# Kernel optimization log

Hardware: AMD Instinct MI355X
Metric: run time of the kernel (lower is better)

## Reference

```python
import jax, jax.numpy as jnp
import numpy as np

N = 50000      # nodes
E = 800000     # edges
P = 200000     # link pairs
D_IN = 128     # input_dim
F_NUM = 128    # filter_num
OUT = 2        # out_dim
K = 10         # APPNP propagation steps
ALPHA = 0.1    # teleport prob


def setup_inputs() -> dict:
    key = jax.random.key(0)
    ks = jax.random.split(key, 9)
    x = jax.random.normal(ks[0], (N, D_IN), dtype=jnp.float32)
    edge_index = jax.random.randint(ks[1], (2, E), 0, N)
    index = jax.random.randint(ks[2], (P, 2), 0, N)
    s1 = 1.0 / np.sqrt(D_IN)
    s2 = 1.0 / np.sqrt(F_NUM)
    s3 = 1.0 / np.sqrt(2 * F_NUM)
    W1 = jax.random.uniform(ks[3], (F_NUM, D_IN), minval=-s1, maxval=s1)
    b1 = jax.random.uniform(ks[4], (F_NUM,), minval=-s1, maxval=s1)
    W2 = jax.random.uniform(ks[5], (F_NUM, F_NUM), minval=-s2, maxval=s2)
    b2 = jax.random.uniform(ks[6], (F_NUM,), minval=-s2, maxval=s2)
    W3 = jax.random.uniform(ks[7], (OUT, 2 * F_NUM), minval=-s3, maxval=s3)
    b3 = jax.random.uniform(ks[8], (OUT,), minval=-s3, maxval=s3)
    return {"x": x, "edge_index": edge_index, "index": index,
            "W1": W1, "b1": b1, "W2": W2, "b2": b2, "W3": W3, "b3": b3}


def _gcn_norm(edge_index, num_nodes):
    # PyG gcn_norm: add self-loops, sym norm D^{-1/2} (A+I) D^{-1/2}
    src, dst = edge_index[0], edge_index[1]
    loop = jnp.arange(num_nodes, dtype=src.dtype)
    src = jnp.concatenate([src, loop])
    dst = jnp.concatenate([dst, loop])
    deg = jax.ops.segment_sum(jnp.ones_like(src, dtype=jnp.float32), dst,
                              num_segments=num_nodes)
    dinv = jnp.where(deg > 0, jax.lax.rsqrt(deg), 0.0)
    norm = dinv[src] * dinv[dst]  # [E+N]
    return src, dst, norm


def _appnp(x, src, dst, norm, num_nodes):
    # h_{k+1} = (1-alpha) * A_hat h_k + alpha * x0
    def step(h, _):
        agg = jax.ops.segment_sum(norm[:, None] * h[src], dst,
                                  num_segments=num_nodes)
        return (1.0 - ALPHA) * agg + ALPHA * x, None
    h, _ = jax.lax.scan(step, x, None, length=K)
    return h


def reference(x, edge_index, index, W1, b1, W2, b2, W3, b3):
    num_nodes = x.shape[0]
    src, dst, norm = _gcn_norm(edge_index, num_nodes)
    h = x @ W1.T + b1                      # [N, F]
    h = jax.nn.relu(_appnp(h, src, dst, norm, num_nodes))
    h = h @ W2.T + b2                      # [N, F]
    h = jax.nn.relu(_appnp(h, src, dst, norm, num_nodes))
    feat = jnp.concatenate([h[index[:, 0]], h[index[:, 1]]], axis=-1)  # [P, 2F]
    out = feat @ W3.T + b3                 # [P, OUT]
    return jax.nn.log_softmax(out, axis=1)
```

## Files before the change

### kernel.cpp

```cpp
#include <hip/hip_runtime.h>
#include <math.h>

#define NN 50000
#define NE 800000
#define NP 200000
#define NF 128
#define NNP (NN + 1)
#define NEDGE_TOT (NE + NN)
#define NBLK 196
#define NBK 64
#define DPB 782
#define BKCAP 16384
#define EPB 2048
#define NSL 4
#define SF 32
#define NCPAD 1000064

typedef __attribute__((ext_vector_type(8))) short short8;
typedef __attribute__((ext_vector_type(4))) float float4v;
typedef __attribute__((ext_vector_type(2))) _Float16 h2;

__device__ __forceinline__ unsigned short f2bf(float f) {
    unsigned u = __float_as_uint(f);
    return (unsigned short)((u + 0x7fffu + ((u >> 16) & 1u)) >> 16);
}
__device__ __forceinline__ unsigned pack2bf(float a, float b) {
    return (unsigned)f2bf(a) | ((unsigned)f2bf(b) << 16);
}

__device__ __forceinline__ h2 u2h2(unsigned u) {
    union { unsigned u; h2 h; } c; c.u = u; return c.h;
}
__device__ __forceinline__ unsigned h22u(h2 h) {
    union { unsigned u; h2 h; } c; c.h = h; return c.u;
}
__device__ __forceinline__ float h_lo(unsigned u) { return (float)u2h2(u).x; }
__device__ __forceinline__ float h_hi(unsigned u) { return (float)u2h2(u).y; }
__device__ __forceinline__ unsigned pack2h(float a, float b) {
    h2 h; h.x = (_Float16)a; h.y = (_Float16)b; return h22u(h);
}

__global__ __launch_bounds__(256) void init_cnt_k(int* __restrict__ cnt,
                                                  float4* __restrict__ puv) {
    int i = blockIdx.x * 256 + threadIdx.x;
    if (i < NN) {
        cnt[i] = 1;
        puv[i] = make_float4(0.f, 0.f, 0.f, 0.f);
    }
}

__global__ __launch_bounds__(256) void count_k(const int* __restrict__ ei,
                                               int* __restrict__ cnt) {
    int e = blockIdx.x * 256 + threadIdx.x;
    if (e < NE) atomicAdd(&cnt[ei[NE + e]], 1);
}

__global__ __launch_bounds__(256) void scan_reduce_k(const int* __restrict__ cnt,
                                                     int* __restrict__ bsum,
                                                     float* __restrict__ dinv) {
    __shared__ int s[256];
    int t = threadIdx.x;
    int idx = blockIdx.x * 256 + t;
    int v = (idx < NN) ? cnt[idx] : 0;
    if (idx < NN) dinv[idx] = rsqrtf((float)v);
    int vp = (v + 3) & ~3;
    s[t] = vp;
    __syncthreads();
    for (int off = 128; off > 0; off >>= 1) {
        if (t < off) s[t] += s[t + off];
        __syncthreads();
    }
    if (t == 0) bsum[blockIdx.x] = s[0];
}

__global__ __launch_bounds__(256) void scan_bsums_k(const int* __restrict__ bsum,
                                                    int* __restrict__ boff) {
    __shared__ int s[256];
    int t = threadIdx.x;
    int v = (t < NBLK) ? bsum[t] : 0;
    s[t] = v;
    __syncthreads();
    for (int off = 1; off < 256; off <<= 1) {
        int add = (t >= off) ? s[t - off] : 0;
        __syncthreads();
        s[t] += add;
        __syncthreads();
    }
    if (t < NBLK) boff[t] = s[t] - v;
}

__global__ __launch_bounds__(256) void scan_down_k(const int* __restrict__ cnt,
                                                   const int* __restrict__ boff,
                                                   int* __restrict__ row_ptr) {
    __shared__ int s[256];
    int t = threadIdx.x;
    int idx = blockIdx.x * 256 + t;
    int v = (idx < NN) ? ((cnt[idx] + 3) & ~3) : 0;
    s[t] = v;
    __syncthreads();
    for (int off = 1; off < 256; off <<= 1) {
        int add = (t >= off) ? s[t - off] : 0;
        __syncthreads();
        s[t] += add;
        __syncthreads();
    }
    int excl = s[t] - v + boff[blockIdx.x] + 4;
    if (idx < NN) {
        row_ptr[idx] = excl;
        if (idx == NN - 1) row_ptr[NN] = excl + v;
    }
}

__global__ __launch_bounds__(256) void fill_cols_k(unsigned* __restrict__ colsu) {
    int t = blockIdx.x * 256 + threadIdx.x;
    if (t < NCPAD / 2) colsu[t] = (unsigned)NN | ((unsigned)NN << 16);
}

__global__ __launch_bounds__(256) void bin_k(const int* __restrict__ ei,
                                             int* __restrict__ gtail,
                                             int2* __restrict__ gbk) {
    __shared__ int cntA[NBK], baseA[NBK], gposA[NBK];
    __shared__ int2 stage[EPB];
    int tid = threadIdx.x;
    int ebase = blockIdx.x * EPB;
    int sv[8], dv[8], lp8[8], bk8[8];
    bool val[8];
    if (tid < NBK) cntA[tid] = 0;
    __syncthreads();
#pragma unroll
    for (int k = 0; k < 8; ++k) {
        int e = ebase + k * 256 + tid;
        val[k] = (e < NEDGE_TOT);
        if (val[k]) {
            int s, d;
            if (e < NE) { s = ei[e]; d = ei[NE + e]; }
            else        { s = d = e - NE; }
            sv[k] = s; dv[k] = d;
            bk8[k] = d / DPB;
            lp8[k] = atomicAdd(&cntA[bk8[k]], 1);
        }
    }
    __syncthreads();
    if (tid == 0) {
        int run = 0;
        for (int b = 0; b < NBK; ++b) { baseA[b] = run; run += cntA[b]; }
    }
    __syncthreads();
    if (tid < NBK && cntA[tid] > 0)
        gposA[tid] = atomicAdd(&gtail[tid], cntA[tid]);
    __syncthreads();
#pragma unroll
    for (int k = 0; k < 8; ++k)
        if (val[k]) {
            int2 r; r.x = sv[k]; r.y = dv[k];
            stage[baseA[bk8[k]] + lp8[k]] = r;
        }
    __syncthreads();
    int total = baseA[NBK - 1] + cntA[NBK - 1];
    for (int i = tid; i < total; i += 256) {
        int2 r = stage[i];
        int b = r.y / DPB;
        gbk[(size_t)b * BKCAP + gposA[b] + (i - baseA[b])] = r;
    }
}

__global__ __launch_bounds__(256) void build_k(const int* __restrict__ row_ptr,
                                               const int* __restrict__ gtail,
                                               const int2* __restrict__ gbk,
                                               unsigned short* __restrict__ cols) {
    __shared__ int wcur[DPB];
    int tid = threadIdx.x;
    int b = blockIdx.x;
    int d0 = b * DPB;
    for (int i = tid; i < DPB; i += 256) {
        int d = d0 + i;
        wcur[i] = (d < NN) ? row_ptr[d] : 0;
    }
    __syncthreads();
    int nb = gtail[b];
    const int2* src = gbk + (size_t)b * BKCAP;
    for (int t = tid; t < nb; t += 256) {
        int2 r = src[t];
        int pos = atomicAdd(&wcur[r.y - d0], 1);
        cols[pos] = (unsigned short)r.x;
    }
}

__global__ __launch_bounds__(256) void zero_k(unsigned short* Ys1, unsigned short* Ys2,
                                              unsigned short* HA, unsigned short* HB,
                                              int* gtail) {
    int t = threadIdx.x;
    unsigned short* bufs[4] = {Ys1, Ys2, HA, HB};
    unsigned short* bp = bufs[t >> 6];
    int s = (t >> 4) & 3, u = t & 15;
    ((unsigned*)(bp + ((size_t)s * NNP + NN) * SF))[u] = 0u;
    if (t < NBK) gtail[t] = 0;
}

__global__ __launch_bounds__(256) void cast_w_k(const float* __restrict__ W,
                                                unsigned short* __restrict__ Wb) {
    int t = blockIdx.x * 256 + threadIdx.x;
    if (t >= 128 * 128 / 8) return;
    int i = t * 8;
    float4 f0 = *(const float4*)(W + i);
    float4 f1 = *(const float4*)(W + i + 4);
    uint4 q;
    q.x = pack2bf(f0.x, f0.y);
    q.y = pack2bf(f0.z, f0.w);
    q.z = pack2bf(f1.x, f1.y);
    q.w = pack2bf(f1.z, f1.w);
    *(uint4*)(Wb + i) = q;
}

#define GPAD 136
template <bool F32IN>
__global__ __launch_bounds__(256) void gemm_mfma_k(const void* __restrict__ Xv,
                                                   const unsigned short* __restrict__ Wb,
                                                   const float* __restrict__ bias,
                                                   const float* __restrict__ dinv,
                                                   unsigned short* __restrict__ Yu,
                                                   unsigned short* __restrict__ Ys,
                                                   int nrows) {
    __shared__ unsigned short sm[4 * 16 * GPAD];
    int wave = threadIdx.x >> 6, lane = threadIdx.x & 63;
    int rbase = blockIdx.x * 64 + wave * 16;
    if (rbase >= nrows) return;
    int quad = lane >> 4, mn = lane & 15;
    float4v acc[8];
#pragma unroll
    for (int ft = 0; ft < 8; ++ft) acc[ft] = (float4v){0.f, 0.f, 0.f, 0.f};
#pragma unroll
    for (int kb = 0; kb < 128; kb += 32) {
        short8 a;
        if (F32IN) {
            const float* X = (const float*)Xv;
            float4 f0 = *(const float4*)(X + (size_t)(rbase + mn) * NF + kb + quad * 8);
            float4 f1 = *(const float4*)(X + (size_t)(rbase + mn) * NF + kb + quad * 8 + 4);
            a[0] = (short)f2bf(f0.x); a[1] = (short)f2bf(f0.y);
            a[2] = (short)f2bf(f0.z); a[3] = (short)f2bf(f0.w);
            a[4] = (short)f2bf(f1.x); a[5] = (short)f2bf(f1.y);
            a[6] = (short)f2bf(f1.z); a[7] = (short)f2bf(f1.w);
        } else {
            const unsigned short* X = (const unsigned short*)Xv;
            a = *(const short8*)(X + (size_t)(rbase + mn) * NF + kb + quad * 8);
        }
#pragma unroll
        for (int ft = 0; ft < 8; ++ft) {
            short8 b = *(const short8*)(Wb + (size_t)(ft * 16 + mn) * NF + kb + quad * 8);
            acc[ft] = __builtin_amdgcn_mfma_f32_16x16x32_bf16(a, b, acc[ft], 0, 0, 0);
        }
    }
    unsigned short* smw = sm + wave * 16 * GPAD;
#pragma unroll
    for (int ft = 0; ft < 8; ++ft) {
        float bv = bias[ft * 16 + mn];
#pragma unroll
        for (int r = 0; r < 4; ++r) {
            union { _Float16 h; unsigned short s; } cv;
            cv.h = (_Float16)(acc[ft][r] + bv);
            smw[(quad * 4 + r) * GPAD + ft * 16 + mn] = cv.s;
        }
    }
    __syncthreads();
#pragma unroll
    for (int t = 0; t < 4; ++t) {
        int rl = t * 4 + quad;
        int row = rbase + rl;
        uint4 q = *(const uint4*)(smw + rl * GPAD + mn * 8);
        size_t sb = ((size_t)(mn >> 2) * NNP + row) * SF + (mn & 3) * 8;
        *(uint4*)(Yu + sb) = q;
        float g = dinv[row];
        uint4 qs;
        qs.x = pack2h(g * h_lo(q.x), g * h_hi(q.x));
        qs.y = pack2h(g * h_lo(q.y), g * h_hi(q.y));
        qs.z = pack2h(g * h_lo(q.z), g * h_hi(q.z));
        qs.w = pack2h(g * h_lo(q.w), g * h_hi(q.w));
        *(uint4*)(Ys + sb) = qs;
    }
}

__global__ __launch_bounds__(512) void appnp_slice_k(
    const unsigned short* __restrict__ hs,
    const unsigned short* __restrict__ x0,
    const float* __restrict__ dinv,
    unsigned short* __restrict__ out,
    const int* __restrict__ row_ptr,
    const unsigned short* __restrict__ cols,
    int mode,
    const float* __restrict__ W3,
    float* __restrict__ puv) {
    int b = blockIdx.x;
    int x = b & 7;
    int s = x & 3, hh = x >> 2;
    int wave = threadIdx.x >> 6, lane = threadIdx.x & 63;
    int g = lane >> 3, fo = lane & 7;
    int wid = (b >> 3) * 128 + hh * 64 + wave * 8 + g;
    bool valid = wid < NN;
    int nid = valid ? wid : NN;
    const unsigned short* hsS = hs + (size_t)s * NNP * SF;
    int beg = 0, dp = 0;
    if (valid) { beg = row_ptr[wid]; dp = row_ptr[wid + 1] - beg; }
    int dpm = dp;
    dpm = max(dpm, __shfl_xor(dpm, 8, 64));
    dpm = max(dpm, __shfl_xor(dpm, 16, 64));
    dpm = max(dpm, __shfl_xor(dpm, 32, 64));
    float gsc = valid ? dinv[wid] : 0.f;
    uint2 xq = *(const uint2*)(x0 + ((size_t)s * NNP + nid) * SF + fo * 4);
    h2 a01; a01.x = (_Float16)0.f; a01.y = (_Float16)0.f;
    h2 a23 = a01;
    if (dpm > 0) {
        int o0 = (0 < dp) ? beg : 0;
        int o1 = (4 < dp) ? beg + 4 : 0;
        ushort4 cq = *(const ushort4*)(cols + o0);
        ushort4 cq1 = *(const ushort4*)(cols + o1);
        uint2 q0 = *(const uint2*)(hsS + (size_t)cq.x * SF + fo * 4);
        uint2 q1 = *(const uint2*)(hsS + (size_t)cq.y * SF + fo * 4);
        uint2 q2 = *(const uint2*)(hsS + (size_t)cq.z * SF + fo * 4);
        uint2 q3 = *(const uint2*)(hsS + (size_t)cq.w * SF + fo * 4);
        for (int j = 0; j < dpm; j += 4) {
            int on = (j + 8 < dp) ? beg + j + 8 : 0;
            ushort4 cq2 = *(const ushort4*)(cols + on);
            uint2 p0 = *(const uint2*)(hsS + (size_t)cq1.x * SF + fo * 4);
            uint2 p1 = *(const uint2*)(hsS + (size_t)cq1.y * SF + fo * 4);
            uint2 p2 = *(const uint2*)(hsS + (size_t)cq1.z * SF + fo * 4);
            uint2 p3 = *(const uint2*)(hsS + (size_t)cq1.w * SF + fo * 4);
            a01 += (u2h2(q0.x) + u2h2(q1.x)) + (u2h2(q2.x) + u2h2(q3.x));
            a23 += (u2h2(q0.y) + u2h2(q1.y)) + (u2h2(q2.y) + u2h2(q3.y));
            q0 = p0; q1 = p1; q2 = p2; q3 = p3;
            cq1 = cq2;
        }
    }
    float s9 = 0.9f * gsc;
    float h0 = s9 * (float)a01.x + 0.1f * h_lo(xq.x);
    float h1 = s9 * (float)a01.y + 0.1f * h_hi(xq.x);
    float h2v = s9 * (float)a23.x + 0.1f * h_lo(xq.y);
    float h3 = s9 * (float)a23.y + 0.1f * h_hi(xq.y);
    if (mode == 0) {
        if (valid) {
            uint2 oq;
            oq.x = pack2h(gsc * h0, gsc * h1);
            oq.y = pack2h(gsc * h2v, gsc * h3);
            *(uint2*)(out + ((size_t)s * NNP + wid) * SF + fo * 4) = oq;
        }
    } else {
        h0 = fmaxf(h0, 0.f); h1 = fmaxf(h1, 0.f);
        h2v = fmaxf(h2v, 0.f); h3 = fmaxf(h3, 0.f);
        if (mode == 1) {
            if (valid) {
                uint2 oq;
                oq.x = pack2bf(h0, h1);
                oq.y = pack2bf(h2v, h3);
                *(uint2*)(out + (size_t)wid * NF + s * SF + fo * 4) = oq;
            }
        } else {
            int fb = s * SF + fo * 4;
            float4 wu0 = *(const float4*)(W3 + fb);
            float4 wv0 = *(const float4*)(W3 + 128 + fb);
            float4 wu1 = *(const float4*)(W3 + 256 + fb);
            float4 wv1 = *(const float4*)(W3 + 384 + fb);
            float du0 = h0 * wu0.x + h1 * wu0.y + h2v * wu0.z + h3 * wu0.w;
            float du1 = h0 * wu1.x + h1 * wu1.y + h2v * wu1.z + h3 * wu1.w;
            float dv0 = h0 * wv0.x + h1 * wv0.y + h2v * wv0.z + h3 * wv0.w;
            float dv1 = h0 * wv1.x + h1 * wv1.y + h2v * wv1.z + h3 * wv1.w;
            du0 += __shfl_xor(du0, 1, 64); du0 += __shfl_xor(du0, 2, 64);
            du0 += __shfl_xor(du0, 4, 64);
            du1 += __shfl_xor(du1, 1, 64); du1 += __shfl_xor(du1, 2, 64);
            du1 += __shfl_xor(du1, 4, 64);
            dv0 += __shfl_xor(dv0, 1, 64); dv0 += __shfl_xor(dv0, 2, 64);
            dv0 += __shfl_xor(dv0, 4, 64);
            dv1 += __shfl_xor(dv1, 1, 64); dv1 += __shfl_xor(dv1, 2, 64);
            dv1 += __shfl_xor(dv1, 4, 64);
            if (valid && fo < 4) {
                float v = (fo == 0) ? du0 : (fo == 1) ? du1
                          : (fo == 2) ? dv0 : dv1;
                atomicAdd(&puv[(size_t)wid * 4 + fo], v);
            }
        }
    }
}

__global__ __launch_bounds__(256) void pair2_k(const float4* __restrict__ puv,
                                               const int2* __restrict__ index,
                                               const float* __restrict__ b3,
                                               float* __restrict__ outp) {
    int p = blockIdx.x * 256 + threadIdx.x;
    if (p >= NP) return;
    int2 uv = index[p];
    float4 a = puv[uv.x];
    float4 b = puv[uv.y];
    float s0 = a.x + b.z + b3[0];
    float s1 = a.y + b.w + b3[1];
    float m = fmaxf(s0, s1);
    float lse = m + logf(expf(s0 - m) + expf(s1 - m));
    *(float2*)(outp + (size_t)p * 2) = make_float2(s0 - lse, s1 - lse);
}

extern "C" void kernel_launch(void* const* d_in, const int* in_sizes, int n_in,
                              void* d_out, int out_size, void* d_ws, size_t ws_size,
                              hipStream_t stream) {
    const float* x  = (const float*)d_in[0];
    const int* ei   = (const int*)d_in[1];
    const int* idx  = (const int*)d_in[2];
    const float* W1 = (const float*)d_in[3];
    const float* b1 = (const float*)d_in[4];
    const float* W2 = (const float*)d_in[5];
    const float* b2 = (const float*)d_in[6];
    const float* W3 = (const float*)d_in[7];
    const float* b3 = (const float*)d_in[8];
    float* out = (float*)d_out;

    char* ws = (char*)d_ws;
    size_t off = 0;
    auto alloc = [&](size_t bytes) -> void* {
        void* p = ws + off;
        off = (off + bytes + 255) & ~(size_t)255;
        return p;
    };
    const size_t HROWS = (size_t)NSL * NNP * SF;
    int*   cnt     = (int*)  alloc(NN * sizeof(int));
    float* dinv    = (float*)alloc(NN * sizeof(float));
    int*   row_ptr = (int*)  alloc((NN + 1) * sizeof(int));
    int*   bsum    = (int*)  alloc(NBLK * sizeof(int));
    int*   boff    = (int*)  alloc(NBLK * sizeof(int));
    int*   gtail   = (int*)  alloc(NBK * sizeof(int));
    int2*  gbk     = (int2*) alloc((size_t)NBK * BKCAP * sizeof(int2));
    unsigned short* cols = (unsigned short*)alloc((size_t)NCPAD * 2);
    float4* puv    = (float4*)alloc((size_t)NN * sizeof(float4));
    unsigned short* Wb1 = (unsigned short*)alloc(128 * 128 * 2);
    unsigned short* Wb2 = (unsigned short*)alloc(128 * 128 * 2);
    unsigned short* Yu1 = (unsigned short*)alloc(HROWS * 2);
    unsigned short* Ys1 = (unsigned short*)alloc(HROWS * 2);
    unsigned short* Yu2 = (unsigned short*)alloc(HROWS * 2);
    unsigned short* Ys2 = (unsigned short*)alloc(HROWS * 2);
    unsigned short* HA  = (unsigned short*)alloc(HROWS * 2);
    unsigned short* HB  = (unsigned short*)alloc(HROWS * 2);
    unsigned short* Hrelu = (unsigned short*)alloc((size_t)NN * NF * 2);

    const int gN    = (NN + 255) / 256;
    const int gE    = (NE + 255) / 256;
    const int gBin  = (NEDGE_TOT + EPB - 1) / EPB;
    const int gGemm = (NN + 63) / 64;
    const int gFill = (NCPAD / 2 + 255) / 256;
    const int gSlice = ((NN + 127) / 128) * 8;
    const int gPair = (NP + 255) / 256;

    cast_w_k<<<8, 256, 0, stream>>>(W1, Wb1);
    cast_w_k<<<8, 256, 0, stream>>>(W2, Wb2);
    zero_k<<<1, 256, 0, stream>>>(Ys1, Ys2, HA, HB, gtail);
    init_cnt_k<<<gN, 256, 0, stream>>>(cnt, puv);
    count_k<<<gE, 256, 0, stream>>>(ei, cnt);
    scan_reduce_k<<<NBLK, 256, 0, stream>>>(cnt, bsum, dinv);
    scan_bsums_k<<<1, 256, 0, stream>>>(bsum, boff);
    scan_down_k<<<NBLK, 256, 0, stream>>>(cnt, boff, row_ptr);
    fill_cols_k<<<gFill, 256, 0, stream>>>((unsigned*)cols);
    bin_k<<<gBin, 256, 0, stream>>>(ei, gtail, gbk);
    build_k<<<NBK, 256, 0, stream>>>(row_ptr, gtail, gbk, cols);

    float* puvf = (float*)puv;
    gemm_mfma_k<true><<<gGemm, 256, 0, stream>>>(x, Wb1, b1, dinv, Yu1, Ys1, NN);
    {
        const unsigned short* cur = Ys1;
        for (int k = 0; k < 10; ++k) {
            unsigned short* dst = (k == 9) ? Hrelu : ((k & 1) ? HB : HA);
            appnp_slice_k<<<gSlice, 512, 0, stream>>>(cur, Yu1, dinv, dst, row_ptr,
                                                      cols, (k == 9) ? 1 : 0, W3, puvf);
            cur = dst;
        }
    }
    gemm_mfma_k<false><<<gGemm, 256, 0, stream>>>(Hrelu, Wb2, b2, dinv, Yu2, Ys2, NN);
    {
        const unsigned short* cur = Ys2;
        for (int k = 0; k < 10; ++k) {
            unsigned short* dst = (k & 1) ? HB : HA;
            appnp_slice_k<<<gSlice, 512, 0, stream>>>(cur, Yu2, dinv, dst, row_ptr,
                                                      cols, (k == 9) ? 2 : 0, W3, puvf);
            cur = dst;
        }
    }
    pair2_k<<<gPair, 256, 0, stream>>>(puv, (const int2*)idx, b3, out);
}
```

Baseline: 827.5 us.

## Split features into 8 slices of 16 and deepen gather prefetch pipeline

Changes the feature-sliced layout from 4 slices of 32 halves to 8 slices of 16, so each node row per slice is 32 bytes. The APPNP kernel now assigns 16 nodes per wave with 4 lanes each instead of 8 nodes with 8 lanes. The gather loop prefetches two groups of neighbor rows ahead instead of one and loads the column indices with nontemporal loads. The smaller slices are meant to improve cache locality for the random gathers and raise memory-level parallelism. In exchange it uses more registers and launches a different block mapping; the edge-loop divergence now spans 16 nodes per wave.

```diff
diff --git a/kernel.cpp b/kernel.cpp
--- a/kernel.cpp
+++ b/kernel.cpp
@@ -12,13 +12,14 @@
 #define DPB 782
 #define BKCAP 16384
 #define EPB 2048
-#define NSL 4
-#define SF 32
+#define NSL 8
+#define SF 16
 #define NCPAD 1000064
 
 typedef __attribute__((ext_vector_type(8))) short short8;
 typedef __attribute__((ext_vector_type(4))) float float4v;
 typedef __attribute__((ext_vector_type(2))) _Float16 h2;
+typedef __attribute__((ext_vector_type(4))) unsigned short us4;
 
 __device__ __forceinline__ unsigned short f2bf(float f) {
     unsigned u = __float_as_uint(f);
@@ -192,7 +193,7 @@
     int t = threadIdx.x;
     unsigned short* bufs[4] = {Ys1, Ys2, HA, HB};
     unsigned short* bp = bufs[t >> 6];
-    int s = (t >> 4) & 3, u = t & 15;
+    int s = (t >> 3) & 7, u = t & 7;
     ((unsigned*)(bp + ((size_t)s * NNP + NN) * SF))[u] = 0u;
     if (t < NBK) gtail[t] = 0;
 }
@@ -267,7 +268,7 @@
         int rl = t * 4 + quad;
         int row = rbase + rl;
         uint4 q = *(const uint4*)(smw + rl * GPAD + mn * 8);
-        size_t sb = ((size_t)(mn >> 2) * NNP + row) * SF + (mn & 3) * 8;
+        size_t sb = ((size_t)(mn >> 1) * NNP + row) * SF + (mn & 1) * 8;
         *(uint4*)(Yu + sb) = q;
         float g = dinv[row];
         uint4 qs;
@@ -290,17 +291,17 @@
     const float* __restrict__ W3,
     float* __restrict__ puv) {
     int b = blockIdx.x;
-    int x = b & 7;
-    int s = x & 3, hh = x >> 2;
+    int s = b & 7;
     int wave = threadIdx.x >> 6, lane = threadIdx.x & 63;
-    int g = lane >> 3, fo = lane & 7;
-    int wid = (b >> 3) * 128 + hh * 64 + wave * 8 + g;
+    int g = lane >> 2, fo = lane & 3;
+    int wid = (b >> 3) * 128 + wave * 16 + g;
     bool valid = wid < NN;
     int nid = valid ? wid : NN;
     const unsigned short* hsS = hs + (size_t)s * NNP * SF;
     int beg = 0, dp = 0;
     if (valid) { beg = row_ptr[wid]; dp = row_ptr[wid + 1] - beg; }
     int dpm = dp;
+    dpm = max(dpm, __shfl_xor(dpm, 4, 64));
     dpm = max(dpm, __shfl_xor(dpm, 8, 64));
     dpm = max(dpm, __shfl_xor(dpm, 16, 64));
     dpm = max(dpm, __shfl_xor(dpm, 32, 64));
@@ -309,25 +310,33 @@
     h2 a01; a01.x = (_Float16)0.f; a01.y = (_Float16)0.f;
     h2 a23 = a01;
     if (dpm > 0) {
-        int o0 = (0 < dp) ? beg : 0;
-        int o1 = (4 < dp) ? beg + 4 : 0;
-        ushort4 cq = *(const ushort4*)(cols + o0);
-        ushort4 cq1 = *(const ushort4*)(cols + o1);
-        uint2 q0 = *(const uint2*)(hsS + (size_t)cq.x * SF + fo * 4);
-        uint2 q1 = *(const uint2*)(hsS + (size_t)cq.y * SF + fo * 4);
-        uint2 q2 = *(const uint2*)(hsS + (size_t)cq.z * SF + fo * 4);
-        uint2 q3 = *(const uint2*)(hsS + (size_t)cq.w * SF + fo * 4);
+        int fb4 = fo * 4;
+        auto colsat = [&](int j4) -> us4 {
+            int o = (j4 < dp) ? beg + j4 : 0;
+            return __builtin_nontemporal_load((const us4*)(cols + o));
+        };
+        us4 c0 = colsat(0);
+        us4 c1 = colsat(4);
+        us4 c2 = colsat(8);
+        uint2 A0 = *(const uint2*)(hsS + (size_t)c0.x * SF + fb4);
+        uint2 A1 = *(const uint2*)(hsS + (size_t)c0.y * SF + fb4);
+        uint2 A2 = *(const uint2*)(hsS + (size_t)c0.z * SF + fb4);
+        uint2 A3 = *(const uint2*)(hsS + (size_t)c0.w * SF + fb4);
+        uint2 B0 = *(const uint2*)(hsS + (size_t)c1.x * SF + fb4);
+        uint2 B1 = *(const uint2*)(hsS + (size_t)c1.y * SF + fb4);
+        uint2 B2 = *(const uint2*)(hsS + (size_t)c1.z * SF + fb4);
+        uint2 B3 = *(const uint2*)(hsS + (size_t)c1.w * SF + fb4);
         for (int j = 0; j < dpm; j += 4) {
-            int on = (j + 8 < dp) ? beg + j + 8 : 0;
-            ushort4 cq2 = *(const ushort4*)(cols + on);
-            uint2 p0 = *(const uint2*)(hsS + (size_t)cq1.x * SF + fo * 4);
-            uint2 p1 = *(const uint2*)(hsS + (size_t)cq1.y * SF + fo * 4);
-            uint2 p2 = *(const uint2*)(hsS + (size_t)cq1.z * SF + fo * 4);
-            uint2 p3 = *(const uint2*)(hsS + (size_t)cq1.w * SF + fo * 4);
-            a01 += (u2h2(q0.x) + u2h2(q1.x)) + (u2h2(q2.x) + u2h2(q3.x));
-            a23 += (u2h2(q0.y) + u2h2(q1.y)) + (u2h2(q2.y) + u2h2(q3.y));
-            q0 = p0; q1 = p1; q2 = p2; q3 = p3;
-            cq1 = cq2;
+            us4 c3 = colsat(j + 12);
+            uint2 C0 = *(const uint2*)(hsS + (size_t)c2.x * SF + fb4);
+            uint2 C1 = *(const uint2*)(hsS + (size_t)c2.y * SF + fb4);
+            uint2 C2 = *(const uint2*)(hsS + (size_t)c2.z * SF + fb4);
+            uint2 C3 = *(const uint2*)(hsS + (size_t)c2.w * SF + fb4);
+            a01 += (u2h2(A0.x) + u2h2(A1.x)) + (u2h2(A2.x) + u2h2(A3.x));
+            a23 += (u2h2(A0.y) + u2h2(A1.y)) + (u2h2(A2.y) + u2h2(A3.y));
+            A0 = B0; A1 = B1; A2 = B2; A3 = B3;
+            B0 = C0; B1 = C1; B2 = C2; B3 = C3;
+            c2 = c3;
         }
     }
     float s9 = 0.9f * gsc;
@@ -363,14 +372,10 @@
             float dv0 = h0 * wv0.x + h1 * wv0.y + h2v * wv0.z + h3 * wv0.w;
             float dv1 = h0 * wv1.x + h1 * wv1.y + h2v * wv1.z + h3 * wv1.w;
             du0 += __shfl_xor(du0, 1, 64); du0 += __shfl_xor(du0, 2, 64);
-            du0 += __shfl_xor(du0, 4, 64);
             du1 += __shfl_xor(du1, 1, 64); du1 += __shfl_xor(du1, 2, 64);
-            du1 += __shfl_xor(du1, 4, 64);
             dv0 += __shfl_xor(dv0, 1, 64); dv0 += __shfl_xor(dv0, 2, 64);
-            dv0 += __shfl_xor(dv0, 4, 64);
             dv1 += __shfl_xor(dv1, 1, 64); dv1 += __shfl_xor(dv1, 2, 64);
-            dv1 += __shfl_xor(dv1, 4, 64);
-            if (valid && fo < 4) {
+            if (valid) {
                 float v = (fo == 0) ? du0 : (fo == 1) ? du1
                           : (fo == 2) ? dv0 : dv1;
                 atomicAdd(&puv[(size_t)wid * 4 + fo], v);
```

New measurement: 1.405 ms. 1.7x slower.
